# Kernel optimization log

Hardware: AMD Instinct MI355X
Metric: run time of the kernel (lower is better)

The kernel has to match this reference:

```python
import jax, jax.numpy as jnp
import numpy as np

NUM_CONN = 8

def _ein_reduce(f):
    # Einstein t-norm fold over last axis: T(a,b) = ab / (2 - (a+b-ab))
    acc = f[..., 0]
    for i in range(1, f.shape[-1]):
        b = f[..., i]
        ab = acc * b
        acc = ab / (2.0 - (acc + b - ab))
    return acc

def _coein_reduce(f):
    # Einstein t-conorm fold over last axis: S(a,b) = (a+b) / (1 + ab)
    acc = f[..., 0]
    for i in range(1, f.shape[-1]):
        b = f[..., i]
        acc = (acc + b) / (1.0 + acc * b)
    return acc

def _ddlg_layer(x, w, idx, is_train):
    # x: [B, in], idx: [out, C] int, w: [out, 4]
    feats = x[:, idx]                      # [B, out, C] gather
    ops = jnp.stack([
        jnp.min(feats, axis=-1),
        jnp.max(feats, axis=-1),
        _ein_reduce(feats),
        _coein_reduce(feats),
    ], axis=-1)                            # [B, out, 4]
    if is_train:
        prob = jax.nn.softmax(w, axis=-1)  # [out, 4]
    else:
        prob = jax.nn.one_hot(jnp.argmax(w, axis=-1), 4, dtype=x.dtype)
    return jnp.einsum('bof,of->bo', ops, prob)

def setup_inputs() -> dict:
    key = jax.random.key(0)
    ks = jax.random.split(key, 6)
    sizes = [4096, 2048, 1024, 2048, 4096]
    x = jax.random.uniform(ks[0], (4096, sizes[0]), dtype=jnp.float32)
    ws = [jax.random.normal(ks[1 + i], (sizes[i + 1], 4), dtype=jnp.float32) for i in range(4)]
    rng = np.random.default_rng(0)
    idxs = []
    for i in range(4):
        # randperm-without-replacement per output neuron
        perm = np.argsort(rng.random((sizes[i + 1], sizes[i])), axis=-1)[:, :NUM_CONN]
        idxs.append(jnp.asarray(perm, dtype=jnp.int32))
    return {
        'x': x,
        'w0': ws[0], 'w1': ws[1], 'w2': ws[2], 'w3': ws[3],
        'idx0': idxs[0], 'idx1': idxs[1], 'idx2': idxs[2], 'idx3': idxs[3],
        'is_train': 1,
    }

def reference(x, w0, w1, w2, w3, idx0, idx1, idx2, idx3, is_train):
    h = _ddlg_layer(x, w0, idx0, is_train)
    h = _ddlg_layer(h, w1, idx1, is_train)
    h = _ddlg_layer(h, w2, idx2, is_train)
    h = _ddlg_layer(h, w3, idx3, is_train)
    return h
```

## Files before the change

kernel.cpp:

```cpp
#include <hip/hip_runtime.h>
#include <hip/hip_bf16.h>


#define BATCH 4096

typedef float    f2 __attribute__((ext_vector_type(2)));
typedef _Float16 h4 __attribute__((ext_vector_type(4)));

__device__ __forceinline__ float fastrcp(float x) { return __builtin_amdgcn_rcpf(x); }

__global__ __launch_bounds__(256) void probs_k(const float* __restrict__ w0,
                                               const float* __restrict__ w1,
                                               const float* __restrict__ w2,
                                               const float* __restrict__ w3,
                                               const int* __restrict__ is_train,
                                               float4* __restrict__ probs) {
    int g = blockIdx.x * 256 + threadIdx.x;
    if (g >= 9216) return;
    const float* w; int o;
    if (g < 2048)      { w = w0; o = g; }
    else if (g < 3072) { w = w1; o = g - 2048; }
    else if (g < 5120) { w = w2; o = g - 3072; }
    else               { w = w3; o = g - 5120; }
    float wv[4];
#pragma unroll
    for (int c = 0; c < 4; ++c) wv[c] = w[(o << 2) + c];
    float p[4];
    if (*is_train) {
        float m = fmaxf(fmaxf(wv[0], wv[1]), fmaxf(wv[2], wv[3]));
        float s = 0.0f;
#pragma unroll
        for (int c = 0; c < 4; ++c) { p[c] = __expf(wv[c] - m); s += p[c]; }
        float inv = fastrcp(s);
#pragma unroll
        for (int c = 0; c < 4; ++c) p[c] *= inv;
    } else {
        int a = 0; float best = wv[0];
#pragma unroll
        for (int c = 1; c < 4; ++c) if (wv[c] > best) { best = wv[c]; a = c; }
#pragma unroll
        for (int c = 0; c < 4; ++c) p[c] = (c == a) ? 1.0f : 0.0f;
    }
    probs[g] = float4{p[0], p[1], p[2], p[3]};
}

__device__ __forceinline__ void gate4(const _Float16* __restrict__ src,
                                      const int4* __restrict__ idx,
                                      const float4* __restrict__ probs,
                                      int o, float r4[4]) {
    const int4 i0 = idx[o * 2];
    const int4 i1 = idx[o * 2 + 1];
    const float4 P = probs[o];
    h4 raw[8];
    raw[0] = *(const h4*)(src + (i0.x << 2));
    raw[1] = *(const h4*)(src + (i0.y << 2));
    raw[2] = *(const h4*)(src + (i0.z << 2));
    raw[3] = *(const h4*)(src + (i0.w << 2));
    raw[4] = *(const h4*)(src + (i1.x << 2));
    raw[5] = *(const h4*)(src + (i1.y << 2));
    raw[6] = *(const h4*)(src + (i1.z << 2));
    raw[7] = *(const h4*)(src + (i1.w << 2));

    h4 mnv = raw[0], mxv = raw[0];
#pragma unroll
    for (int c = 1; c < 8; ++c) {
        mnv = __builtin_elementwise_min(mnv, raw[c]);
        mxv = __builtin_elementwise_max(mxv, raw[c]);
    }

#pragma unroll
    for (int q = 0; q < 2; ++q) {
        f2 v0 = f2{(float)raw[0][2 * q], (float)raw[0][2 * q + 1]};
        f2 De = v0, Ne = 2.0f - v0;
        f2 Nc = 1.0f + v0, Dc = 1.0f - v0;
#pragma unroll
        for (int c = 1; c < 8; ++c) {
            f2 v = f2{(float)raw[c][2 * q], (float)raw[c][2 * q + 1]};
            De *= v;
            Ne *= (2.0f - v);
            Nc += Nc * v;
            Dc -= Dc * v;
        }
        f2 s1 = Ne + De, s2 = Nc + Dc, d1 = Nc - Dc;
        float r0 = fastrcp(s1.x * s2.x);
        float r1 = fastrcp(s1.y * s2.y);
        float einx = (2.0f * De.x * s2.x) * r0;
        float einy = (2.0f * De.y * s2.y) * r1;
        float coex = (d1.x * s1.x) * r0;
        float coey = (d1.y * s1.y) * r1;
        r4[2 * q]     = P.x * (float)mnv[2 * q]     + P.y * (float)mxv[2 * q]     + P.z * einx + P.w * coex;
        r4[2 * q + 1] = P.x * (float)mnv[2 * q + 1] + P.y * (float)mxv[2 * q + 1] + P.z * einy + P.w * coey;
    }
}

__device__ __forceinline__ void layer_pass(const _Float16* __restrict__ src,
                                           _Float16* __restrict__ dst,
                                           const int4* __restrict__ idx,
                                           const float4* __restrict__ probs,
                                           int o) {
    float r4[4];
    gate4(src, idx, probs, o, r4);
    h4 res;
#pragma unroll
    for (int i = 0; i < 4; ++i) res[i] = (_Float16)r4[i];
    *(h4*)(dst + (o << 2)) = res;
}

__global__ __launch_bounds__(1024, 8) void ddlg_fused(const float* __restrict__ x,
                                                      const float4* __restrict__ probs,
                                                      const int4* __restrict__ idx0,
                                                      const int4* __restrict__ idx1,
                                                      const int4* __restrict__ idx2,
                                                      const int4* __restrict__ idx3,
                                                      float* __restrict__ out) {
    __shared__ __align__(16) _Float16 lds[24576];
    const int t  = threadIdx.x;
    const int b0 = blockIdx.x << 2;

    const _Float16* xl = lds;
    _Float16*       h0 = lds + 16384;
    _Float16*       h1 = lds;
    _Float16*       h2 = lds + 16384;

#pragma unroll
    for (int c = 0; c < 4; ++c) {
        const int j = (c << 10) + t;
        const float v0 = x[(size_t)(b0 + 0) * 4096 + j];
        const float v1 = x[(size_t)(b0 + 1) * 4096 + j];
        const float v2 = x[(size_t)(b0 + 2) * 4096 + j];
        const float v3 = x[(size_t)(b0 + 3) * 4096 + j];
        h4 hv;
        hv[0] = (_Float16)v0; hv[1] = (_Float16)v1;
        hv[2] = (_Float16)v2; hv[3] = (_Float16)v3;
        *(h4*)(lds + (j << 2)) = hv;
    }
    __syncthreads();

    layer_pass(xl, h0, idx0, probs, t);
    layer_pass(xl, h0, idx0, probs, t + 1024);
    __syncthreads();

    layer_pass(h0, h1, idx1, probs + 2048, t);
    __syncthreads();

    layer_pass(h1, h2, idx2, probs + 3072, t);
    layer_pass(h1, h2, idx2, probs + 3072, t + 1024);
    __syncthreads();

#pragma unroll
    for (int p = 0; p < 4; ++p) {
        const int o = (p << 10) + t;
        float r4[4];
        gate4(h2, idx3, probs + 5120, o, r4);
#pragma unroll
        for (int b = 0; b < 4; ++b)
            out[(size_t)(b0 + b) * 4096 + o] = r4[b];
    }
}

extern "C" void kernel_launch(void* const* d_in, const int* in_sizes, int n_in,
                              void* d_out, int out_size, void* d_ws, size_t ws_size,
                              hipStream_t stream) {
    const float* x        = (const float*)d_in[0];
    const float* w0       = (const float*)d_in[1];
    const float* w1       = (const float*)d_in[2];
    const float* w2       = (const float*)d_in[3];
    const float* w3       = (const float*)d_in[4];
    const int4*  idx0     = (const int4*)d_in[5];
    const int4*  idx1     = (const int4*)d_in[6];
    const int4*  idx2     = (const int4*)d_in[7];
    const int4*  idx3     = (const int4*)d_in[8];
    const int*   is_train = (const int*)d_in[9];
    float*       out      = (float*)d_out;

    float4* probs = (float4*)d_ws;

    probs_k<<<36, 256, 0, stream>>>(w0, w1, w2, w3, is_train, probs);
    ddlg_fused<<<1024, 1024, 0, stream>>>(x, probs, idx0, idx1, idx2, idx3, out);
}
```

Before: 173.1 us.

## Compute gate math in packed fp16 and pre-scale indices in prep kernel

Moves the whole per-gate computation (min/max, Einstein t-norm/conorm products, reciprocals, weighted mix) from fp32 pairs to packed half4 arithmetic, and stores the gate probabilities as fp16. A combined prep kernel also pre-multiplies the connection indices by 4 into a workspace buffer, which removes shifts in the hot loop and folds four index pointers into one. The aim is to double ALU throughput with packed fp16 and cut instruction count. The cost is lower precision in the products and reciprocals, which could lose accuracy, particularly in the 8-way Einstein products and in fp16 rcp.

```diff
diff --git a/kernel.cpp b/kernel.cpp
--- a/kernel.cpp
+++ b/kernel.cpp
@@ -4,114 +4,131 @@
 
 #define BATCH 4096
 
-typedef float    f2 __attribute__((ext_vector_type(2)));
 typedef _Float16 h4 __attribute__((ext_vector_type(4)));
 
 __device__ __forceinline__ float fastrcp(float x) { return __builtin_amdgcn_rcpf(x); }
+__device__ __forceinline__ _Float16 hrcp(_Float16 x) {
+#if __has_builtin(__builtin_amdgcn_rcph)
+    return __builtin_amdgcn_rcph(x);
+#else
+    return (_Float16)__builtin_amdgcn_rcpf((float)x);
+#endif
+}
+__device__ __forceinline__ h4 splat(_Float16 s) { h4 v = {s, s, s, s}; return v; }
 
-__global__ __launch_bounds__(256) void probs_k(const float* __restrict__ w0,
-                                               const float* __restrict__ w1,
-                                               const float* __restrict__ w2,
-                                               const float* __restrict__ w3,
-                                               const int* __restrict__ is_train,
-                                               float4* __restrict__ probs) {
-    int g = blockIdx.x * 256 + threadIdx.x;
-    if (g >= 9216) return;
-    const float* w; int o;
-    if (g < 2048)      { w = w0; o = g; }
-    else if (g < 3072) { w = w1; o = g - 2048; }
-    else if (g < 5120) { w = w2; o = g - 3072; }
-    else               { w = w3; o = g - 5120; }
-    float wv[4];
+__global__ __launch_bounds__(256) void prep_k(const float* __restrict__ w0,
+                                              const float* __restrict__ w1,
+                                              const float* __restrict__ w2,
+                                              const float* __restrict__ w3,
+                                              const int* __restrict__ is_train,
+                                              const int4* __restrict__ idx0,
+                                              const int4* __restrict__ idx1,
+                                              const int4* __restrict__ idx2,
+                                              const int4* __restrict__ idx3,
+                                              h4* __restrict__ probsH,
+                                              int4* __restrict__ idxS) {
+    const int blk = blockIdx.x;
+    if (blk < 36) {
+        int g = blk * 256 + threadIdx.x;
+        if (g >= 9216) return;
+        const float* w; int o;
+        if (g < 2048)      { w = w0; o = g; }
+        else if (g < 3072) { w = w1; o = g - 2048; }
+        else if (g < 5120) { w = w2; o = g - 3072; }
+        else               { w = w3; o = g - 5120; }
+        float wv[4];
 #pragma unroll
-    for (int c = 0; c < 4; ++c) wv[c] = w[(o << 2) + c];
-    float p[4];
-    if (*is_train) {
-        float m = fmaxf(fmaxf(wv[0], wv[1]), fmaxf(wv[2], wv[3]));
-        float s = 0.0f;
+        for (int c = 0; c < 4; ++c) wv[c] = w[(o << 2) + c];
+        float p[4];
+        if (*is_train) {
+            float m = fmaxf(fmaxf(wv[0], wv[1]), fmaxf(wv[2], wv[3]));
+            float s = 0.0f;
 #pragma unroll
-        for (int c = 0; c < 4; ++c) { p[c] = __expf(wv[c] - m); s += p[c]; }
-        float inv = fastrcp(s);
+            for (int c = 0; c < 4; ++c) { p[c] = __expf(wv[c] - m); s += p[c]; }
+            float inv = fastrcp(s);
 #pragma unroll
-        for (int c = 0; c < 4; ++c) p[c] *= inv;
+            for (int c = 0; c < 4; ++c) p[c] *= inv;
+        } else {
+            int a = 0; float best = wv[0];
+#pragma unroll
+            for (int c = 1; c < 4; ++c) if (wv[c] > best) { best = wv[c]; a = c; }
+#pragma unroll
+            for (int c = 0; c < 4; ++c) p[c] = (c == a) ? 1.0f : 0.0f;
+        }
+        probsH[g] = h4{(_Float16)p[0], (_Float16)p[1], (_Float16)p[2], (_Float16)p[3]};
     } else {
-        int a = 0; float best = wv[0];
-#pragma unroll
-        for (int c = 1; c < 4; ++c) if (wv[c] > best) { best = wv[c]; a = c; }
-#pragma unroll
-        for (int c = 0; c < 4; ++c) p[c] = (c == a) ? 1.0f : 0.0f;
+        int g = (blk - 36) * 256 + threadIdx.x;
+        const int4* src; int off;
+        if (g < 4096)       { src = idx0; off = g; }
+        else if (g < 6144)  { src = idx1; off = g - 4096; }
+        else if (g < 10240) { src = idx2; off = g - 6144; }
+        else                { src = idx3; off = g - 10240; }
+        int4 v = src[off];
+        idxS[g] = int4{v.x << 2, v.y << 2, v.z << 2, v.w << 2};
     }
-    probs[g] = float4{p[0], p[1], p[2], p[3]};
 }
 
-__device__ __forceinline__ void gate4(const _Float16* __restrict__ src,
-                                      const int4* __restrict__ idx,
-                                      const float4* __restrict__ probs,
-                                      int o, float r4[4]) {
+__device__ __forceinline__ h4 gate4h(const _Float16* __restrict__ src,
+                                     const int4* __restrict__ idx,
+                                     const h4* __restrict__ probs,
+                                     int o) {
     const int4 i0 = idx[o * 2];
     const int4 i1 = idx[o * 2 + 1];
-    const float4 P = probs[o];
+    const h4 P = probs[o];
     h4 raw[8];
-    raw[0] = *(const h4*)(src + (i0.x << 2));
-    raw[1] = *(const h4*)(src + (i0.y << 2));
-    raw[2] = *(const h4*)(src + (i0.z << 2));
-    raw[3] = *(const h4*)(src + (i0.w << 2));
-    raw[4] = *(const h4*)(src + (i1.x << 2));
-    raw[5] = *(const h4*)(src + (i1.y << 2));
-    raw[6] = *(const h4*)(src + (i1.z << 2));
-    raw[7] = *(const h4*)(src + (i1.w << 2));
+    raw[0] = *(const h4*)(src + i0.x);
+    raw[1] = *(const h4*)(src + i0.y);
+    raw[2] = *(const h4*)(src + i0.z);
+    raw[3] = *(const h4*)(src + i0.w);
+    raw[4] = *(const h4*)(src + i1.x);
+    raw[5] = *(const h4*)(src + i1.y);
+    raw[6] = *(const h4*)(src + i1.z);
+    raw[7] = *(const h4*)(src + i1.w);
 
-    h4 mnv = raw[0], mxv = raw[0];
+    const h4 one = splat((_Float16)1.0f);
+    const h4 two = splat((_Float16)2.0f);
+
+    h4 mn = raw[0], mx = raw[0], De = raw[0];
+    h4 Ne = two - raw[0];
+    h4 Nc = one + raw[0];
+    h4 Dc = one - raw[0];
 #pragma unroll
     for (int c = 1; c < 8; ++c) {
-        mnv = __builtin_elementwise_min(mnv, raw[c]);
-        mxv = __builtin_elementwise_max(mxv, raw[c]);
+        h4 v = raw[c];
+        mn = __builtin_elementwise_min(mn, v);
+        mx = __builtin_elementwise_max(mx, v);
+        De *= v;
+        Ne *= (two - v);
+        Nc += Nc * v;
+        Dc -= Dc * v;
     }
-
+    h4 s1 = Ne + De;
+    h4 s2 = Nc + Dc;
+    h4 d1 = Nc - Dc;
+    h4 r1, r2;
 #pragma unroll
-    for (int q = 0; q < 2; ++q) {
-        f2 v0 = f2{(float)raw[0][2 * q], (float)raw[0][2 * q + 1]};
-        f2 De = v0, Ne = 2.0f - v0;
-        f2 Nc = 1.0f + v0, Dc = 1.0f - v0;
-#pragma unroll
-        for (int c = 1; c < 8; ++c) {
-            f2 v = f2{(float)raw[c][2 * q], (float)raw[c][2 * q + 1]};
-            De *= v;
-            Ne *= (2.0f - v);
-            Nc += Nc * v;
-            Dc -= Dc * v;
-        }
-        f2 s1 = Ne + De, s2 = Nc + Dc, d1 = Nc - Dc;
-        float r0 = fastrcp(s1.x * s2.x);
-        float r1 = fastrcp(s1.y * s2.y);
-        float einx = (2.0f * De.x * s2.x) * r0;
-        float einy = (2.0f * De.y * s2.y) * r1;
-        float coex = (d1.x * s1.x) * r0;
-        float coey = (d1.y * s1.y) * r1;
-        r4[2 * q]     = P.x * (float)mnv[2 * q]     + P.y * (float)mxv[2 * q]     + P.z * einx + P.w * coex;
-        r4[2 * q + 1] = P.x * (float)mnv[2 * q + 1] + P.y * (float)mxv[2 * q + 1] + P.z * einy + P.w * coey;
-    }
+    for (int e = 0; e < 4; ++e) { r1[e] = hrcp(s1[e]); r2[e] = hrcp(s2[e]); }
+    h4 ein = (De + De) * r1;
+    h4 coe = d1 * r2;
+    h4 res = splat(P[0]) * mn;
+    res += splat(P[1]) * mx;
+    res += splat(P[2]) * ein;
+    res += splat(P[3]) * coe;
+    return res;
 }
 
 __device__ __forceinline__ void layer_pass(const _Float16* __restrict__ src,
                                            _Float16* __restrict__ dst,
                                            const int4* __restrict__ idx,
-                                           const float4* __restrict__ probs,
+                                           const h4* __restrict__ probs,
                                            int o) {
-    float r4[4];
-    gate4(src, idx, probs, o, r4);
-    h4 res;
-#pragma unroll
-    for (int i = 0; i < 4; ++i) res[i] = (_Float16)r4[i];
-    *(h4*)(dst + (o << 2)) = res;
+    h4 r = gate4h(src, idx, probs, o);
+    *(h4*)(dst + (o << 2)) = r;
 }
 
 __global__ __launch_bounds__(1024, 8) void ddlg_fused(const float* __restrict__ x,
-                                                      const float4* __restrict__ probs,
-                                                      const int4* __restrict__ idx0,
-                                                      const int4* __restrict__ idx1,
-                                                      const int4* __restrict__ idx2,
-                                                      const int4* __restrict__ idx3,
+                                                      const h4* __restrict__ probsH,
+                                                      const int4* __restrict__ idxS,
                                                       float* __restrict__ out) {
     __shared__ __align__(16) _Float16 lds[24576];
     const int t  = threadIdx.x;
@@ -136,25 +153,24 @@
     }
     __syncthreads();
 
-    layer_pass(xl, h0, idx0, probs, t);
-    layer_pass(xl, h0, idx0, probs, t + 1024);
+    layer_pass(xl, h0, idxS, probsH, t);
+    layer_pass(xl, h0, idxS, probsH, t + 1024);
     __syncthreads();
 
-    layer_pass(h0, h1, idx1, probs + 2048, t);
+    layer_pass(h0, h1, idxS + 4096, probsH + 2048, t);
     __syncthreads();
 
-    layer_pass(h1, h2, idx2, probs + 3072, t);
-    layer_pass(h1, h2, idx2, probs + 3072, t + 1024);
+    layer_pass(h1, h2, idxS + 6144, probsH + 3072, t);
+    layer_pass(h1, h2, idxS + 6144, probsH + 3072, t + 1024);
     __syncthreads();
 
 #pragma unroll
     for (int p = 0; p < 4; ++p) {
         const int o = (p << 10) + t;
-        float r4[4];
-        gate4(h2, idx3, probs + 5120, o, r4);
+        h4 r = gate4h(h2, idxS + 10240, probsH + 5120, o);
 #pragma unroll
         for (int b = 0; b < 4; ++b)
-            out[(size_t)(b0 + b) * 4096 + o] = r4[b];
+            out[(size_t)(b0 + b) * 4096 + o] = (float)r[b];
     }
 }
 
@@ -173,8 +189,10 @@
     const int*   is_train = (const int*)d_in[9];
     float*       out      = (float*)d_out;
 
-    float4* probs = (float4*)d_ws;
+    h4*   probsH = (h4*)d_ws;
+    int4* idxS   = (int4*)((char*)d_ws + (128 << 10));
 
-    probs_k<<<36, 256, 0, stream>>>(w0, w1, w2, w3, is_train, probs);
-    ddlg_fused<<<1024, 1024, 0, stream>>>(x, probs, idx0, idx1, idx2, idx3, out);
+    prep_k<<<108, 256, 0, stream>>>(w0, w1, w2, w3, is_train,
+                                    idx0, idx1, idx2, idx3, probsH, idxS);
+    ddlg_fused<<<1024, 1024, 0, stream>>>(x, probsH, idxS, out);
 }
```

New measurement: 164.5 us. -5.0%, faster.
